# Kernel optimization log

Hardware: AMD Instinct MI355X
Metric: run time of the kernel (lower is better)

The kernel has to match this reference:

```python
import jax, jax.numpy as jnp
import numpy as np

TANH_EPS = 1e-06
LOG2PI = float(np.log(2.0 * np.pi))


def _atanh(x):
    x = jnp.clip(x, -1.0 + TANH_EPS, 1.0 - TANH_EPS)
    return 0.5 * (jnp.log1p(x) - jnp.log1p(-x))


def setup_inputs() -> dict:
    key = jax.random.key(0)
    ks = jax.random.split(key, 12)
    T, B, O, H, A = 256, 1024, 128, 128, 8
    s = 0.05
    return {
        "obs_seq": jax.random.normal(ks[0], (T, B, O), jnp.float32),
        "actions_seq": jax.random.uniform(ks[1], (T, B, A), jnp.float32, -0.99, 0.99),
        "dones_seq": (jax.random.uniform(ks[2], (T, B)) < 0.02).astype(jnp.float32),
        "h0": jnp.zeros((B, H), jnp.float32),
        "c0": jnp.zeros((B, H), jnp.float32),
        "enc_w1": s * jax.random.normal(ks[3], (H, O), jnp.float32),
        "enc_b1": jnp.zeros((H,), jnp.float32),
        "enc_w2": s * jax.random.normal(ks[4], (H, H), jnp.float32),
        "enc_b2": jnp.zeros((H,), jnp.float32),
        "w_ih": s * jax.random.normal(ks[5], (4 * H, H), jnp.float32),
        "w_hh": s * jax.random.normal(ks[6], (4 * H, H), jnp.float32),
        "b_ih": jnp.zeros((4 * H,), jnp.float32),
        "b_hh": jnp.zeros((4 * H,), jnp.float32),
        "am_w": 0.01 * jax.random.normal(ks[7], (A, H), jnp.float32),
        "am_b": jnp.zeros((A,), jnp.float32),
        "actor_logstd": jnp.zeros((A,), jnp.float32),
        "cr_w": s * jax.random.normal(ks[8], (1, H), jnp.float32),
        "cr_b": jnp.zeros((1,), jnp.float32),
    }


def reference(obs_seq, actions_seq, dones_seq, h0, c0,
              enc_w1, enc_b1, enc_w2, enc_b2,
              w_ih, w_hh, b_ih, b_hh,
              am_w, am_b, actor_logstd, cr_w, cr_b):
    # Encoder (batched over all timesteps): two tanh MLP layers.
    x = jnp.tanh(jnp.einsum('tbo,ho->tbh', obs_seq, enc_w1) + enc_b1)
    x = jnp.tanh(jnp.einsum('tbh,gh->tbg', x, enc_w2) + enc_b2)
    # Precompute input contribution to gates: [T, B, 4H]
    xg = jnp.einsum('tbh,gh->tbg', x, w_ih) + b_ih

    def step(carry, inp):
        h, c = carry
        xg_t, d_t = inp
        m = (1.0 - d_t)[:, None]  # done-masking reset
        h = h * m
        c = c * m
        g = xg_t + h @ w_hh.T + b_hh
        i, f, gg, o = jnp.split(g, 4, axis=-1)
        c2 = jax.nn.sigmoid(f) * c + jax.nn.sigmoid(i) * jnp.tanh(gg)
        h2 = jax.nn.sigmoid(o) * jnp.tanh(c2)
        return (h2, c2), h2

    (hT, cT), ys = jax.lax.scan(step, (h0, c0), (xg, dones_seq))  # ys: [T, B, H]

    values = (jnp.einsum('tbh,vh->tbv', ys, cr_w) + cr_b)[..., 0]  # [T, B]
    mean = jnp.einsum('tbh,ah->tba', ys, am_w) + am_b  # [T, B, A]
    logstd = actor_logstd  # [A]
    u = _atanh(actions_seq)
    # Normal log-prob per dim, summed over action dims
    z = (u - mean) * jnp.exp(-logstd)
    lp_gauss = jnp.sum(-0.5 * z * z - logstd - 0.5 * LOG2PI, axis=-1)
    log_jac = jnp.sum(jnp.log(1.0 - actions_seq ** 2 + TANH_EPS), axis=-1)
    logprobs = lp_gauss - log_jac
    entropies = jnp.sum(0.5 + 0.5 * LOG2PI + logstd) + log_jac
    return logprobs, entropies, values, hT, cT
```

## Files before the change

kernel.cpp:

```cpp
#include <hip/hip_runtime.h>

typedef float f32x4 __attribute__((ext_vector_type(4)));
typedef short short8 __attribute__((ext_vector_type(8)));
typedef short s16x4 __attribute__((ext_vector_type(4)));

#define MFMA16(a, b, c) __builtin_amdgcn_mfma_f32_16x16x32_bf16((a), (b), (c), 0, 0, 0)

#define T_ 256
#define B_ 1024
#define H_ 128
#define TB_ 262144
#define BH_ 131072
#define LOG2PI_F 1.8378770664093453f

__device__ inline short f2bf(float f) {
    unsigned u = __builtin_bit_cast(unsigned, f);
    u += 0x7fffu + ((u >> 16) & 1u);
    return (short)(u >> 16);
}
__device__ inline float bf2f(short s) {
    unsigned u = ((unsigned)(unsigned short)s) << 16;
    return __builtin_bit_cast(float, u);
}
__device__ inline float fexp(float x) { return __builtin_amdgcn_exp2f(x * 1.4426950408889634f); }
__device__ inline float fsigm(float x) { return __builtin_amdgcn_rcpf(1.f + fexp(-x)); }
__device__ inline float ftanh(float x) { return 1.f - 2.f * __builtin_amdgcn_rcpf(fexp(2.f * x) + 1.f); }

__global__ __launch_bounds__(256) void prep_kernel(
    const float* __restrict__ w1, const float* __restrict__ w2,
    const float* __restrict__ wih, const float* __restrict__ whh,
    const float* __restrict__ amw, const float* __restrict__ crw,
    short* __restrict__ w1b, short* __restrict__ w2b,
    short* __restrict__ wihb, short* __restrict__ whhb,
    short* __restrict__ headw)
{
    int i = blockIdx.x * blockDim.x + threadIdx.x;
    if (i < 16384) { w1b[i] = f2bf(w1[i]); w2b[i] = f2bf(w2[i]); }
    wihb[i] = f2bf(wih[i]);
    whhb[i] = f2bf(whh[i]);
    if (i < 2048) {
        int j = i >> 7, k = i & 127;
        float v = (j == 0) ? crw[k] : (j <= 8 ? amw[(j - 1) * 128 + k] : 0.f);
        headw[i] = f2bf(v);
    }
}

__global__ __launch_bounds__(512, 4) void ex_kernel(
    const float* __restrict__ obs, const float* __restrict__ eb1,
    const float* __restrict__ eb2,
    const short* __restrict__ w1b, const short* __restrict__ w2b,
    short* __restrict__ x2p)
{
    __shared__ __align__(16) short xtA[64 * 128];
    __shared__ __align__(16) short xtB[64 * 128];
    __shared__ __align__(16) short xtC[64 * 128];
    const int tid = threadIdx.x;
    const int l = tid & 63, w = tid >> 6;
    const int l15 = l & 15, kg = l >> 4;
    const int srow = tid >> 3, sln = tid & 7;
    const int ssw = (srow & 7) << 3;

    short8 fw1[4], fw2[4];
#pragma unroll
    for (int kk = 0; kk < 4; ++kk) {
        fw1[kk] = *(const short8*)&w1b[(w * 16 + l15) * 128 + kk * 32 + 8 * kg];
        fw2[kk] = *(const short8*)&w2b[(w * 16 + l15) * 128 + kk * 32 + 8 * kg];
        asm volatile("" : "+v"(fw1[kk]), "+v"(fw2[kk]));
    }
    const float bb1 = eb1[w * 16 + l15], bb2 = eb2[w * 16 + l15];

    const int NT = 8;
    const int t0 = blockIdx.x * NT;

    {
        const float* src = obs + ((size_t)t0 * 64 + srow) * 128 + sln * 16;
#pragma unroll
        for (int ii = 0; ii < 2; ++ii) {
            float4 v0 = *(const float4*)(src + ii * 8);
            float4 v1 = *(const float4*)(src + ii * 8 + 4);
            short8 p;
            p[0] = f2bf(v0.x); p[1] = f2bf(v0.y); p[2] = f2bf(v0.z); p[3] = f2bf(v0.w);
            p[4] = f2bf(v1.x); p[5] = f2bf(v1.y); p[6] = f2bf(v1.z); p[7] = f2bf(v1.w);
            *(short8*)(xtA + srow * 128 + ((sln * 16 + ii * 8) ^ ssw)) = p;
        }
    }
    __syncthreads();

    for (int i = 0; i < NT; ++i) {
        const int tile = t0 + i;
        short* bufO = (i & 1) ? xtB : xtA;
        short* bufN = (i & 1) ? xtA : xtB;

        float4 pf[4];
        {
            const int tn = (i + 1 < NT) ? tile + 1 : tile;
            const float* src = obs + ((size_t)tn * 64 + srow) * 128 + sln * 16;
#pragma unroll
            for (int ii = 0; ii < 4; ++ii) pf[ii] = *(const float4*)(src + ii * 4);
        }

#pragma unroll
        for (int mf = 0; mf < 4; ++mf) {
            const int ra = mf * 16 + l15, swa = (ra & 7) << 3;
            short8 a[4];
#pragma unroll
            for (int kk = 0; kk < 4; ++kk)
                a[kk] = *(const short8*)&bufO[ra * 128 + ((kk * 32 + 8 * kg) ^ swa)];
            f32x4 acc = {bb1, bb1, bb1, bb1};
#pragma unroll
            for (int kk = 0; kk < 4; ++kk) acc = MFMA16(a[kk], fw1[kk], acc);
#pragma unroll
            for (int j = 0; j < 4; ++j) {
                int rw = mf * 16 + kg * 4 + j;
                xtC[rw * 128 + ((w * 16 + l15) ^ ((rw & 7) << 3))] = f2bf(ftanh(acc[j]));
            }
        }
        __syncthreads();

        const int t = (tile * 64) >> 10;
        const int b_base = (tile * 64) & 1023;
#pragma unroll
        for (int mf = 0; mf < 4; ++mf) {
            const int ra = mf * 16 + l15, swa = (ra & 7) << 3;
            short8 a[4];
#pragma unroll
            for (int kk = 0; kk < 4; ++kk)
                a[kk] = *(const short8*)&xtC[ra * 128 + ((kk * 32 + 8 * kg) ^ swa)];
            f32x4 acc = {bb2, bb2, bb2, bb2};
#pragma unroll
            for (int kk = 0; kk < 4; ++kk) acc = MFMA16(a[kk], fw2[kk], acc);
#pragma unroll
            for (int j = 0; j < 4; ++j) {
                int b = b_base + mf * 16 + kg * 4 + j;
                size_t idx = (((size_t)t * 256 + (b >> 2)) * 4 + (b & 3)) * 128 + w * 16 + l15;
                x2p[idx] = f2bf(ftanh(acc[j]));
            }
        }
#pragma unroll
        for (int ii = 0; ii < 2; ++ii) {
            float4 v0 = pf[ii * 2], v1 = pf[ii * 2 + 1];
            short8 p;
            p[0] = f2bf(v0.x); p[1] = f2bf(v0.y); p[2] = f2bf(v0.z); p[3] = f2bf(v0.w);
            p[4] = f2bf(v1.x); p[5] = f2bf(v1.y); p[6] = f2bf(v1.z); p[7] = f2bf(v1.w);
            *(short8*)(bufN + srow * 128 + ((sln * 16 + ii * 8) ^ ssw)) = p;
        }
        __syncthreads();
    }
}

__global__ __launch_bounds__(512) void lstm_kernel(
    const short* __restrict__ x2p, const short* __restrict__ whhb,
    const short* __restrict__ wihb,
    const float* __restrict__ h0, const float* __restrict__ c0,
    const float* __restrict__ bhh, const float* __restrict__ bih,
    const float* __restrict__ dones,
    short* __restrict__ ys, float* __restrict__ out)
{
    __shared__ __align__(16) short hbuf[2][4 * 160];
    __shared__ __align__(16) short x2b[2][16 * 160];
    __shared__ float dlds[1028];
    const int tid = threadIdx.x;
    const int l = tid & 63, w = tid >> 6;
    const int l15 = l & 15, kg = l >> 4;
    const int b0 = blockIdx.x * 4;
    const int d = w * 16 + l15;
    const int blk = blockIdx.x;
    const int xsw = (l15 & 7) << 3;

    short8 bfr[4][4], bfi[4][4];
#pragma unroll
    for (int s = 0; s < 4; ++s)
#pragma unroll
        for (int kk = 0; kk < 4; ++kk) {
            bfr[s][kk] = *(const short8*)&whhb[(s * 128 + d) * 128 + kk * 32 + 8 * kg];
            bfi[s][kk] = *(const short8*)&wihb[(s * 128 + d) * 128 + kk * 32 + 8 * kg];
            asm volatile("" : "+v"(bfr[s][kk]), "+v"(bfi[s][kk]));
        }

    for (int i = tid; i < 1028; i += 512) {
        int t = i >> 2, jj = i & 3;
        dlds[i] = (t < 256) ? 1.f - dones[t * 1024 + b0 + jj] : 1.f;
    }

    float bh[4];
#pragma unroll
    for (int s = 0; s < 4; ++s) bh[s] = bhh[s * 128 + d] + bih[s * 128 + d];

    const int st_toff = tid >> 7, st_j = (tid >> 5) & 3, st_dim = (tid & 31) * 4;
    const int st_row = st_j * 4 + st_toff;
    const int xrow160 = st_row * 160 + (st_dim ^ ((st_row & 7) << 3));
#define X2GIDX(G) ((((size_t)(((G) * 4 + st_toff) <= 255 ? ((G) * 4 + st_toff) : 255) * 256 + blk) * 4 + st_j) * 128 + st_dim)

    {
        s16x4 v0 = *(const s16x4*)(x2p + X2GIDX(0));
        s16x4 v1 = *(const s16x4*)(x2p + X2GIDX(1));
        *(s16x4*)&x2b[0][xrow160] = v0;
        *(s16x4*)&x2b[1][xrow160] = v1;
    }
    s16x4 xpf = *(const s16x4*)(x2p + X2GIDX(2));
    asm volatile("s_waitcnt lgkmcnt(0)" ::: "memory");
    __syncthreads();

    f32x4 xgA[4], xgB[4];
#pragma unroll
    for (int s = 0; s < 4; ++s) {
        short8 ax[4];
#pragma unroll
        for (int kk = 0; kk < 4; ++kk)
            ax[kk] = *(const short8*)&x2b[0][l15 * 160 + ((kk * 32 + kg * 8) ^ xsw)];
        f32x4 accX = {bh[s], bh[s], bh[s], bh[s]};
#pragma unroll
        for (int kk = 0; kk < 4; ++kk) accX = MFMA16(ax[kk], bfi[s][kk], accX);
        xgA[s] = accX;
    }

    float h = h0[(b0 + kg) * 128 + d];
    float c = c0[(b0 + kg) * 128 + d];
    hbuf[0][kg * 160 + d] = f2bf(h * dlds[kg]);
    asm volatile("s_waitcnt lgkmcnt(0)" ::: "memory");
    __syncthreads();

    const int aoff = (l15 >> 2) * 160;
    float mreg = dlds[kg];

#define LSTM_STEP(t, hb, i_s, xgC, xgN, x2R, DO_T3, GNEXT)                                 \
    {                                                                                      \
        short8 a[4];                                                                       \
        _Pragma("unroll")                                                                  \
        for (int kk = 0; kk < 4; ++kk)                                                     \
            a[kk] = *(const short8*)&hbuf[hb][aoff + kk * 32 + kg * 8];                    \
        f32x4 acc[4];                                                                      \
        _Pragma("unroll")                                                                  \
        for (int s = 0; s < 4; ++s) acc[s] = f32x4{0.f, 0.f, 0.f, 0.f};                    \
        _Pragma("unroll")                                                                  \
        for (int kk = 0; kk < 4; ++kk)                                                     \
            _Pragma("unroll")                                                              \
            for (int s = 0; s < 4; ++s) acc[s] = MFMA16(a[kk], bfr[s][kk], acc[s]);        \
        {                       \
            short8 ax[4];                                                                  \
            _Pragma("unroll")                                                              \
            for (int kk = 0; kk < 4; ++kk)                                                 \
                ax[kk] = *(const short8*)&x2R[l15 * 160 + ((kk * 32 + kg * 8) ^ xsw)];     \
            const float bhx = bh[i_s];                                                     \
            f32x4 accX = {bhx, bhx, bhx, bhx};                                             \
            _Pragma("unroll")                                                              \
            for (int kk = 0; kk < 4; ++kk) accX = MFMA16(ax[kk], bfi[i_s][kk], accX);      \
            xgN[i_s] = accX;                                                               \
        }                                                                                  \
        if (DO_T3) {                                                                      \
            *(s16x4*)&x2W[xrow160] = xpf;                                                  \
            xpf = *(const s16x4*)(x2p + X2GIDX(GNEXT));                                    \
        }                                                                                  \
        float mn = dlds[((t) + 1) * 4 + kg];                                               \
        float gi = acc[0][0] + xgC[0][i_s];                                                \
        float gf = acc[1][0] + xgC[1][i_s];                                                \
        float gg = acc[2][0] + xgC[2][i_s];                                                \
        float go = acc[3][0] + xgC[3][i_s];                                                \
        c = fsigm(gf) * (c * mreg) + fsigm(gi) * ftanh(gg);                                \
        float h2 = fsigm(go) * ftanh(c);                                                   \
        h = h2;                                                                            \
        mreg = mn;                                                                         \
        hbuf[(hb) ^ 1][kg * 160 + d] = f2bf(h2 * mn);                                      \
        ys[((size_t)(t) * 1024 + b0 + kg) * 128 + d] = f2bf(h2);                           \
        asm volatile("s_waitcnt lgkmcnt(0)" ::: "memory");                                 \
        __builtin_amdgcn_s_barrier();                                                      \
        asm volatile("" ::: "memory");                                                     \
    }

    for (int g = 0; g < 64; g += 2) {
        {
            const int tb = g * 4;
            const short* x2R = &x2b[1][0];
            short* x2W = &x2b[0][0];
            LSTM_STEP(tb + 0, 0, 0, xgA, xgB, x2R, 0, 0);
            LSTM_STEP(tb + 1, 1, 1, xgA, xgB, x2R, 0, 0);
            LSTM_STEP(tb + 2, 0, 2, xgA, xgB, x2R, 0, 0);
            LSTM_STEP(tb + 3, 1, 3, xgA, xgB, x2R, 1, (g + 3));
        }
        {
            const int tb = (g + 1) * 4;
            const short* x2R = &x2b[0][0];
            short* x2W = &x2b[1][0];
            LSTM_STEP(tb + 0, 0, 0, xgB, xgA, x2R, 0, 0);
            LSTM_STEP(tb + 1, 1, 1, xgB, xgA, x2R, 0, 0);
            LSTM_STEP(tb + 2, 0, 2, xgB, xgA, x2R, 0, 0);
            LSTM_STEP(tb + 3, 1, 3, xgB, xgA, x2R, 1, (g + 4));
        }
    }
#undef LSTM_STEP
#undef X2GIDX

    out[3 * TB_ + (b0 + kg) * 128 + d] = h;
    out[3 * TB_ + BH_ + (b0 + kg) * 128 + d] = c;
}

__global__ __launch_bounds__(256) void head_kernel(
    const short* __restrict__ ys, const short* __restrict__ headw,
    const float* __restrict__ crb, const float* __restrict__ amb,
    const float* __restrict__ lstd, const float* __restrict__ actions,
    float* __restrict__ out)
{
    __shared__ float heads[256][12];
    const int tid = threadIdx.x;
    const int l = tid & 63, w = tid >> 6;
    const int l15 = l & 15, kg = l >> 4;
    const int rr0 = blockIdx.x * 256;
    const int rw0 = rr0 + w * 64;

    short8 bb[4];
#pragma unroll
    for (int kk = 0; kk < 4; ++kk)
        bb[kk] = *(const short8*)&headw[l15 * 128 + kk * 32 + 8 * kg];
    const float bias = (l15 == 0) ? crb[0] : (l15 <= 8 ? amb[l15 - 1] : 0.f);

#pragma unroll
    for (int rt = 0; rt < 4; ++rt) {
        const short* src = ys + (size_t)(rw0 + rt * 16 + l15) * 128;
        short8 a[4];
#pragma unroll
        for (int kk = 0; kk < 4; ++kk)
            a[kk] = *(const short8*)(src + kk * 32 + 8 * kg);
        f32x4 acc = {bias, bias, bias, bias};
#pragma unroll
        for (int kk = 0; kk < 4; ++kk) acc = MFMA16(a[kk], bb[kk], acc);
        if (l15 < 9) {
#pragma unroll
            for (int j = 0; j < 4; ++j)
                heads[w * 64 + rt * 16 + kg * 4 + j][l15] = acc[j];
        }
    }
    asm volatile("s_waitcnt lgkmcnt(0)" ::: "memory");

    const int r = rw0 + l;
    const float* hp = heads[w * 64 + l];
    const float* ap = actions + (size_t)r * 8;
    float4 a0 = *(const float4*)(ap);
    float4 a1 = *(const float4*)(ap + 4);
    float lp = 0.f, lj = 0.f, entS = 0.f;
#pragma unroll
    for (int ai = 0; ai < 8; ++ai) {
        float x = (ai < 4) ? ((ai == 0) ? a0.x : (ai == 1) ? a0.y : (ai == 2) ? a0.z : a0.w)
                           : ((ai == 4) ? a1.x : (ai == 5) ? a1.y : (ai == 6) ? a1.z : a1.w);
        float xc = fminf(fmaxf(x, -1.f + 1e-6f), 1.f - 1e-6f);
        float u = 0.5f * logf((1.f + xc) / (1.f - xc));
        float ls = lstd[ai];
        float z = (u - hp[1 + ai]) * expf(-ls);
        lp += -0.5f * z * z - ls;
        lj += logf(1.f - x * x + 1e-6f);
        entS += ls;
    }
    lp -= 8.f * 0.5f * LOG2PI_F;
    entS += 8.f * (0.5f + 0.5f * LOG2PI_F);
    out[r] = lp - lj;
    out[TB_ + r] = entS + lj;
    out[2 * TB_ + r] = hp[0];
}

extern "C" void kernel_launch(void* const* d_in, const int* in_sizes, int n_in,
                              void* d_out, int out_size, void* d_ws, size_t ws_size,
                              hipStream_t stream) {
    const float* obs   = (const float*)d_in[0];
    const float* acts  = (const float*)d_in[1];
    const float* dones = (const float*)d_in[2];
    const float* h0    = (const float*)d_in[3];
    const float* c0    = (const float*)d_in[4];
    const float* w1    = (const float*)d_in[5];
    const float* b1    = (const float*)d_in[6];
    const float* w2    = (const float*)d_in[7];
    const float* b2    = (const float*)d_in[8];
    const float* wih   = (const float*)d_in[9];
    const float* whh   = (const float*)d_in[10];
    const float* bih   = (const float*)d_in[11];
    const float* bhh   = (const float*)d_in[12];
    const float* amw   = (const float*)d_in[13];
    const float* amb   = (const float*)d_in[14];
    const float* lstd  = (const float*)d_in[15];
    const float* crw   = (const float*)d_in[16];
    const float* crb   = (const float*)d_in[17];
    float* out = (float*)d_out;

    char* ws = (char*)d_ws;
    short* w1b   = (short*)(ws + 0);
    short* w2b   = (short*)(ws + 32768);
    short* wihb  = (short*)(ws + 65536);
    short* whhb  = (short*)(ws + 196608);
    short* headw = (short*)(ws + 327680);
    short* x2p   = (short*)(ws + 524288);
    short* ysb   = (short*)(ws + 524288 + 67108864);
    if (ws_size < (size_t)524288 + 67108864 + 67108864) return;

    hipLaunchKernelGGL(prep_kernel, dim3(256), dim3(256), 0, stream,
                       w1, w2, wih, whh, amw, crw, w1b, w2b, wihb, whhb, headw);
    hipLaunchKernelGGL(ex_kernel, dim3(512), dim3(512), 0, stream,
                       obs, b1, b2, w1b, w2b, x2p);
    hipLaunchKernelGGL(lstm_kernel, dim3(256), dim3(512), 0, stream,
                       x2p, whhb, wihb, h0, c0, bhh, bih, dones, ysb, out);
    hipLaunchKernelGGL(head_kernel, dim3(1024), dim3(256), 0, stream,
                       ysb, headw, crb, amb, lstd, acts, out);
}
```

Measured before the change: 228.8 us.

## Fuse head projection into LSTM loop and drop weight prep kernel

Removes the separate weight-conversion kernel by converting fp32 weights to bf16 inline at kernel start. The LSTM kernel keeps recent hidden states in an LDS ring buffer and computes the critic/actor head MFMA on them, delayed by a few steps, writing a compact 12-float head buffer. This replaces the full bf16 ys write and re-read by a separate head kernel. The recurrent accumulator is now seeded with the precomputed input gates instead of adding them afterward. The trade-off is extra MFMA and LDS work inside the serial recurrence, plus more LDS use per block.

```diff
diff --git a/kernel.cpp b/kernel.cpp
--- a/kernel.cpp
+++ b/kernel.cpp
@@ -18,37 +18,21 @@
     u += 0x7fffu + ((u >> 16) & 1u);
     return (short)(u >> 16);
 }
-__device__ inline float bf2f(short s) {
-    unsigned u = ((unsigned)(unsigned short)s) << 16;
-    return __builtin_bit_cast(float, u);
-}
 __device__ inline float fexp(float x) { return __builtin_amdgcn_exp2f(x * 1.4426950408889634f); }
 __device__ inline float fsigm(float x) { return __builtin_amdgcn_rcpf(1.f + fexp(-x)); }
 __device__ inline float ftanh(float x) { return 1.f - 2.f * __builtin_amdgcn_rcpf(fexp(2.f * x) + 1.f); }
 
-__global__ __launch_bounds__(256) void prep_kernel(
-    const float* __restrict__ w1, const float* __restrict__ w2,
-    const float* __restrict__ wih, const float* __restrict__ whh,
-    const float* __restrict__ amw, const float* __restrict__ crw,
-    short* __restrict__ w1b, short* __restrict__ w2b,
-    short* __restrict__ wihb, short* __restrict__ whhb,
-    short* __restrict__ headw)
-{
-    int i = blockIdx.x * blockDim.x + threadIdx.x;
-    if (i < 16384) { w1b[i] = f2bf(w1[i]); w2b[i] = f2bf(w2[i]); }
-    wihb[i] = f2bf(wih[i]);
-    whhb[i] = f2bf(whh[i]);
-    if (i < 2048) {
-        int j = i >> 7, k = i & 127;
-        float v = (j == 0) ? crw[k] : (j <= 8 ? amw[(j - 1) * 128 + k] : 0.f);
-        headw[i] = f2bf(v);
-    }
+__device__ inline short8 pack8(float4 u0, float4 u1) {
+    short8 p;
+    p[0] = f2bf(u0.x); p[1] = f2bf(u0.y); p[2] = f2bf(u0.z); p[3] = f2bf(u0.w);
+    p[4] = f2bf(u1.x); p[5] = f2bf(u1.y); p[6] = f2bf(u1.z); p[7] = f2bf(u1.w);
+    return p;
 }
 
 __global__ __launch_bounds__(512, 4) void ex_kernel(
     const float* __restrict__ obs, const float* __restrict__ eb1,
     const float* __restrict__ eb2,
-    const short* __restrict__ w1b, const short* __restrict__ w2b,
+    const float* __restrict__ w1f, const float* __restrict__ w2f,
     short* __restrict__ x2p)
 {
     __shared__ __align__(16) short xtA[64 * 128];
@@ -63,8 +47,10 @@
     short8 fw1[4], fw2[4];
 #pragma unroll
     for (int kk = 0; kk < 4; ++kk) {
-        fw1[kk] = *(const short8*)&w1b[(w * 16 + l15) * 128 + kk * 32 + 8 * kg];
-        fw2[kk] = *(const short8*)&w2b[(w * 16 + l15) * 128 + kk * 32 + 8 * kg];
+        const float* s1 = w1f + (w * 16 + l15) * 128 + kk * 32 + 8 * kg;
+        const float* s2 = w2f + (w * 16 + l15) * 128 + kk * 32 + 8 * kg;
+        fw1[kk] = pack8(*(const float4*)s1, *(const float4*)(s1 + 4));
+        fw2[kk] = pack8(*(const float4*)s2, *(const float4*)(s2 + 4));
         asm volatile("" : "+v"(fw1[kk]), "+v"(fw2[kk]));
     }
     const float bb1 = eb1[w * 16 + l15], bb2 = eb2[w * 16 + l15];
@@ -78,10 +64,7 @@
         for (int ii = 0; ii < 2; ++ii) {
             float4 v0 = *(const float4*)(src + ii * 8);
             float4 v1 = *(const float4*)(src + ii * 8 + 4);
-            short8 p;
-            p[0] = f2bf(v0.x); p[1] = f2bf(v0.y); p[2] = f2bf(v0.z); p[3] = f2bf(v0.w);
-            p[4] = f2bf(v1.x); p[5] = f2bf(v1.y); p[6] = f2bf(v1.z); p[7] = f2bf(v1.w);
-            *(short8*)(xtA + srow * 128 + ((sln * 16 + ii * 8) ^ ssw)) = p;
+            *(short8*)(xtA + srow * 128 + ((sln * 16 + ii * 8) ^ ssw)) = pack8(v0, v1);
         }
     }
     __syncthreads();
@@ -138,25 +121,25 @@
         }
 #pragma unroll
         for (int ii = 0; ii < 2; ++ii) {
-            float4 v0 = pf[ii * 2], v1 = pf[ii * 2 + 1];
-            short8 p;
-            p[0] = f2bf(v0.x); p[1] = f2bf(v0.y); p[2] = f2bf(v0.z); p[3] = f2bf(v0.w);
-            p[4] = f2bf(v1.x); p[5] = f2bf(v1.y); p[6] = f2bf(v1.z); p[7] = f2bf(v1.w);
-            *(short8*)(bufN + srow * 128 + ((sln * 16 + ii * 8) ^ ssw)) = p;
+            *(short8*)(bufN + srow * 128 + ((sln * 16 + ii * 8) ^ ssw)) =
+                pack8(pf[ii * 2], pf[ii * 2 + 1]);
         }
         __syncthreads();
     }
 }
 
 __global__ __launch_bounds__(512) void lstm_kernel(
-    const short* __restrict__ x2p, const short* __restrict__ whhb,
-    const short* __restrict__ wihb,
+    const short* __restrict__ x2p, const float* __restrict__ whh,
+    const float* __restrict__ wih,
     const float* __restrict__ h0, const float* __restrict__ c0,
     const float* __restrict__ bhh, const float* __restrict__ bih,
     const float* __restrict__ dones,
-    short* __restrict__ ys, float* __restrict__ out)
+    const float* __restrict__ amw, const float* __restrict__ crw,
+    const float* __restrict__ amb, const float* __restrict__ crb,
+    float* __restrict__ headbuf, float* __restrict__ out)
 {
     __shared__ __align__(16) short hbuf[2][4 * 160];
+    __shared__ __align__(16) short hring[16 * 640];
     __shared__ __align__(16) short x2b[2][16 * 160];
     __shared__ float dlds[1028];
     const int tid = threadIdx.x;
@@ -172,10 +155,28 @@
     for (int s = 0; s < 4; ++s)
 #pragma unroll
         for (int kk = 0; kk < 4; ++kk) {
-            bfr[s][kk] = *(const short8*)&whhb[(s * 128 + d) * 128 + kk * 32 + 8 * kg];
-            bfi[s][kk] = *(const short8*)&wihb[(s * 128 + d) * 128 + kk * 32 + 8 * kg];
+            const float* sr = whh + ((s * 128 + d) * 128 + kk * 32 + 8 * kg);
+            const float* si = wih + ((s * 128 + d) * 128 + kk * 32 + 8 * kg);
+            bfr[s][kk] = pack8(*(const float4*)sr, *(const float4*)(sr + 4));
+            bfi[s][kk] = pack8(*(const float4*)si, *(const float4*)(si + 4));
             asm volatile("" : "+v"(bfr[s][kk]), "+v"(bfi[s][kk]));
         }
+
+    short8 hb4[4];
+#pragma unroll
+    for (int kk = 0; kk < 4; ++kk) {
+        if (l15 == 0) {
+            const float* s0 = crw + kk * 32 + 8 * kg;
+            hb4[kk] = pack8(*(const float4*)s0, *(const float4*)(s0 + 4));
+        } else if (l15 <= 8) {
+            const float* s0 = amw + (l15 - 1) * 128 + kk * 32 + 8 * kg;
+            hb4[kk] = pack8(*(const float4*)s0, *(const float4*)(s0 + 4));
+        } else {
+            hb4[kk] = short8{0, 0, 0, 0, 0, 0, 0, 0};
+        }
+        asm volatile("" : "+v"(hb4[kk]));
+    }
+    const float biasH = (l15 == 0) ? crb[0] : (l15 <= 8 ? amb[l15 - 1] : 0.f);
 
     for (int i = tid; i < 1028; i += 512) {
         int t = i >> 2, jj = i & 3;
@@ -223,7 +224,7 @@
     const int aoff = (l15 >> 2) * 160;
     float mreg = dlds[kg];
 
-#define LSTM_STEP(t, hb, i_s, xgC, xgN, x2R, DO_T3, GNEXT)                                 \
+#define LSTM_STEP(t, hb, i_s, xgC, xgN, x2R, DO_T3, GNEXT, DO_HEAD)                        \
     {                                                                                      \
         short8 a[4];                                                                       \
         _Pragma("unroll")                                                                  \
@@ -231,37 +232,48 @@
             a[kk] = *(const short8*)&hbuf[hb][aoff + kk * 32 + kg * 8];                    \
         f32x4 acc[4];                                                                      \
         _Pragma("unroll")                                                                  \
-        for (int s = 0; s < 4; ++s) acc[s] = f32x4{0.f, 0.f, 0.f, 0.f};                    \
+        for (int s = 0; s < 4; ++s) acc[s] = xgC[s];                                       \
         _Pragma("unroll")                                                                  \
         for (int kk = 0; kk < 4; ++kk)                                                     \
             _Pragma("unroll")                                                              \
             for (int s = 0; s < 4; ++s) acc[s] = MFMA16(a[kk], bfr[s][kk], acc[s]);        \
-        {                       \
+        {           \
             short8 ax[4];                                                                  \
             _Pragma("unroll")                                                              \
             for (int kk = 0; kk < 4; ++kk)                                                 \
                 ax[kk] = *(const short8*)&x2R[l15 * 160 + ((kk * 32 + kg * 8) ^ xsw)];     \
-            const float bhx = bh[i_s];                                                     \
-            f32x4 accX = {bhx, bhx, bhx, bhx};                                             \
+            f32x4 accX = {bh[i_s], bh[i_s], bh[i_s], bh[i_s]};                             \
             _Pragma("unroll")                                                              \
             for (int kk = 0; kk < 4; ++kk) accX = MFMA16(ax[kk], bfi[i_s][kk], accX);      \
             xgN[i_s] = accX;                                                               \
+        }                                                                                  \
+        if (DO_HEAD) {                 \
+            int th = (t) - 8 + w;                                                          \
+            const short* hr = &hring[(th & 15) * 640];                                     \
+            short8 ah[4];                                                                  \
+            _Pragma("unroll")                                                              \
+            for (int kk = 0; kk < 4; ++kk)                                                 \
+                ah[kk] = *(const short8*)&hr[aoff + kk * 32 + kg * 8];                     \
+            f32x4 aH = {biasH, biasH, biasH, biasH};                                       \
+            _Pragma("unroll")                                                              \
+            for (int kk = 0; kk < 4; ++kk) aH = MFMA16(ah[kk], hb4[kk], aH);               \
+            if (l15 < 9) headbuf[(th * 1024 + b0 + kg) * 12 + l15] = aH[0];                \
         }                                                                                  \
         if (DO_T3) {                                                                      \
             *(s16x4*)&x2W[xrow160] = xpf;                                                  \
             xpf = *(const s16x4*)(x2p + X2GIDX(GNEXT));                                    \
         }                                                                                  \
         float mn = dlds[((t) + 1) * 4 + kg];                                               \
-        float gi = acc[0][0] + xgC[0][i_s];                                                \
-        float gf = acc[1][0] + xgC[1][i_s];                                                \
-        float gg = acc[2][0] + xgC[2][i_s];                                                \
-        float go = acc[3][0] + xgC[3][i_s];                                                \
+        float gi = acc[0][i_s];                                                            \
+        float gf = acc[1][i_s];                                                            \
+        float gg = acc[2][i_s];                                                            \
+        float go = acc[3][i_s];                                                            \
         c = fsigm(gf) * (c * mreg) + fsigm(gi) * ftanh(gg);                                \
         float h2 = fsigm(go) * ftanh(c);                                                   \
         h = h2;                                                                            \
         mreg = mn;                                                                         \
         hbuf[(hb) ^ 1][kg * 160 + d] = f2bf(h2 * mn);                                      \
-        ys[((size_t)(t) * 1024 + b0 + kg) * 128 + d] = f2bf(h2);                           \
+        hring[((t) & 15) * 640 + kg * 160 + d] = f2bf(h2);                                 \
         asm volatile("s_waitcnt lgkmcnt(0)" ::: "memory");                                 \
         __builtin_amdgcn_s_barrier();                                                      \
         asm volatile("" ::: "memory");                                                     \
@@ -272,79 +284,63 @@
             const int tb = g * 4;
             const short* x2R = &x2b[1][0];
             short* x2W = &x2b[0][0];
-            LSTM_STEP(tb + 0, 0, 0, xgA, xgB, x2R, 0, 0);
-            LSTM_STEP(tb + 1, 1, 1, xgA, xgB, x2R, 0, 0);
-            LSTM_STEP(tb + 2, 0, 2, xgA, xgB, x2R, 0, 0);
-            LSTM_STEP(tb + 3, 1, 3, xgA, xgB, x2R, 1, (g + 3));
+            LSTM_STEP(tb + 0, 0, 0, xgA, xgB, x2R, 0, 0, (g > 0));
+            LSTM_STEP(tb + 1, 1, 1, xgA, xgB, x2R, 0, 0, 0);
+            LSTM_STEP(tb + 2, 0, 2, xgA, xgB, x2R, 0, 0, 0);
+            LSTM_STEP(tb + 3, 1, 3, xgA, xgB, x2R, 1, (g + 3), 0);
         }
         {
             const int tb = (g + 1) * 4;
             const short* x2R = &x2b[0][0];
             short* x2W = &x2b[1][0];
-            LSTM_STEP(tb + 0, 0, 0, xgB, xgA, x2R, 0, 0);
-            LSTM_STEP(tb + 1, 1, 1, xgB, xgA, x2R, 0, 0);
-            LSTM_STEP(tb + 2, 0, 2, xgB, xgA, x2R, 0, 0);
-            LSTM_STEP(tb + 3, 1, 3, xgB, xgA, x2R, 1, (g + 4));
+            LSTM_STEP(tb + 0, 0, 0, xgB, xgA, x2R, 0, 0, 0);
+            LSTM_STEP(tb + 1, 1, 1, xgB, xgA, x2R, 0, 0, 0);
+            LSTM_STEP(tb + 2, 0, 2, xgB, xgA, x2R, 0, 0, 0);
+            LSTM_STEP(tb + 3, 1, 3, xgB, xgA, x2R, 1, (g + 4), 0);
         }
     }
 #undef LSTM_STEP
 #undef X2GIDX
 
+    {
+        int th = 248 + w;
+        const short* hr = &hring[(th & 15) * 640];
+        short8 ah[4];
+#pragma unroll
+        for (int kk = 0; kk < 4; ++kk)
+            ah[kk] = *(const short8*)&hr[aoff + kk * 32 + kg * 8];
+        f32x4 aH = {biasH, biasH, biasH, biasH};
+#pragma unroll
+        for (int kk = 0; kk < 4; ++kk) aH = MFMA16(ah[kk], hb4[kk], aH);
+        if (l15 < 9) headbuf[(th * 1024 + b0 + kg) * 12 + l15] = aH[0];
+    }
+
     out[3 * TB_ + (b0 + kg) * 128 + d] = h;
     out[3 * TB_ + BH_ + (b0 + kg) * 128 + d] = c;
 }
 
-__global__ __launch_bounds__(256) void head_kernel(
-    const short* __restrict__ ys, const short* __restrict__ headw,
-    const float* __restrict__ crb, const float* __restrict__ amb,
-    const float* __restrict__ lstd, const float* __restrict__ actions,
-    float* __restrict__ out)
+__global__ __launch_bounds__(256) void headepi_kernel(
+    const float* __restrict__ headbuf, const float* __restrict__ lstd,
+    const float* __restrict__ actions, float* __restrict__ out)
 {
-    __shared__ float heads[256][12];
-    const int tid = threadIdx.x;
-    const int l = tid & 63, w = tid >> 6;
-    const int l15 = l & 15, kg = l >> 4;
-    const int rr0 = blockIdx.x * 256;
-    const int rw0 = rr0 + w * 64;
-
-    short8 bb[4];
-#pragma unroll
-    for (int kk = 0; kk < 4; ++kk)
-        bb[kk] = *(const short8*)&headw[l15 * 128 + kk * 32 + 8 * kg];
-    const float bias = (l15 == 0) ? crb[0] : (l15 <= 8 ? amb[l15 - 1] : 0.f);
-
-#pragma unroll
-    for (int rt = 0; rt < 4; ++rt) {
-        const short* src = ys + (size_t)(rw0 + rt * 16 + l15) * 128;
-        short8 a[4];
-#pragma unroll
-        for (int kk = 0; kk < 4; ++kk)
-            a[kk] = *(const short8*)(src + kk * 32 + 8 * kg);
-        f32x4 acc = {bias, bias, bias, bias};
-#pragma unroll
-        for (int kk = 0; kk < 4; ++kk) acc = MFMA16(a[kk], bb[kk], acc);
-        if (l15 < 9) {
-#pragma unroll
-            for (int j = 0; j < 4; ++j)
-                heads[w * 64 + rt * 16 + kg * 4 + j][l15] = acc[j];
-        }
-    }
-    asm volatile("s_waitcnt lgkmcnt(0)" ::: "memory");
-
-    const int r = rw0 + l;
-    const float* hp = heads[w * 64 + l];
+    const int r = blockIdx.x * 256 + threadIdx.x;
+    const float* hp = headbuf + (size_t)r * 12;
+    float4 m0 = *(const float4*)(hp);
+    float4 m1 = *(const float4*)(hp + 4);
+    float4 m2 = *(const float4*)(hp + 8);
     const float* ap = actions + (size_t)r * 8;
     float4 a0 = *(const float4*)(ap);
     float4 a1 = *(const float4*)(ap + 4);
+    float mean[8] = {m0.y, m0.z, m0.w, m1.x, m1.y, m1.z, m1.w, m2.x};
+    float act[8] = {a0.x, a0.y, a0.z, a0.w, a1.x, a1.y, a1.z, a1.w};
     float lp = 0.f, lj = 0.f, entS = 0.f;
 #pragma unroll
     for (int ai = 0; ai < 8; ++ai) {
-        float x = (ai < 4) ? ((ai == 0) ? a0.x : (ai == 1) ? a0.y : (ai == 2) ? a0.z : a0.w)
-                           : ((ai == 4) ? a1.x : (ai == 5) ? a1.y : (ai == 6) ? a1.z : a1.w);
+        float x = act[ai];
         float xc = fminf(fmaxf(x, -1.f + 1e-6f), 1.f - 1e-6f);
         float u = 0.5f * logf((1.f + xc) / (1.f - xc));
         float ls = lstd[ai];
-        float z = (u - hp[1 + ai]) * expf(-ls);
+        float z = (u - mean[ai]) * expf(-ls);
         lp += -0.5f * z * z - ls;
         lj += logf(1.f - x * x + 1e-6f);
         entS += ls;
@@ -353,7 +349,7 @@
     entS += 8.f * (0.5f + 0.5f * LOG2PI_F);
     out[r] = lp - lj;
     out[TB_ + r] = entS + lj;
-    out[2 * TB_ + r] = hp[0];
+    out[2 * TB_ + r] = m0.x;
 }
 
 extern "C" void kernel_launch(void* const* d_in, const int* in_sizes, int n_in,
@@ -380,21 +376,14 @@
     float* out = (float*)d_out;
 
     char* ws = (char*)d_ws;
-    short* w1b   = (short*)(ws + 0);
-    short* w2b   = (short*)(ws + 32768);
-    short* wihb  = (short*)(ws + 65536);
-    short* whhb  = (short*)(ws + 196608);
-    short* headw = (short*)(ws + 327680);
-    short* x2p   = (short*)(ws + 524288);
-    short* ysb   = (short*)(ws + 524288 + 67108864);
-    if (ws_size < (size_t)524288 + 67108864 + 67108864) return;
-
-    hipLaunchKernelGGL(prep_kernel, dim3(256), dim3(256), 0, stream,
-                       w1, w2, wih, whh, amw, crw, w1b, w2b, wihb, whhb, headw);
+    short* x2p = (short*)(ws);
+    float* hbf = (float*)(ws + 67108864);
+    if (ws_size < (size_t)67108864 + 12582912) return;
+
     hipLaunchKernelGGL(ex_kernel, dim3(512), dim3(512), 0, stream,
-                       obs, b1, b2, w1b, w2b, x2p);
+                       obs, b1, b2, w1, w2, x2p);
     hipLaunchKernelGGL(lstm_kernel, dim3(256), dim3(512), 0, stream,
-                       x2p, whhb, wihb, h0, c0, bhh, bih, dones, ysb, out);
-    hipLaunchKernelGGL(head_kernel, dim3(1024), dim3(256), 0, stream,
-                       ysb, headw, crb, amb, lstd, acts, out);
-}
+                       x2p, whh, wih, h0, c0, bhh, bih, dones, amw, crw, amb, crb, hbf, out);
+    hipLaunchKernelGGL(headepi_kernel, dim3(1024), dim3(256), 0, stream,
+                       hbf, lstd, acts, out);
+}
```

After: 216.2 us. 1.06x faster.
